# Optimization experiments

Hardware: AMD Instinct MI355X
Metric: run time of the kernel (lower is better)

Reference implementation:

```python
import jax, jax.numpy as jnp
import numpy as np

B, T, D, H = 2, 2048, 2048, 16
DH = D // H

def setup_inputs() -> dict:
    key = jax.random.key(0)
    k1, k2, k3 = jax.random.split(key, 3)
    x = jax.random.normal(k1, (B, T, D), dtype=jnp.float32)
    w_qkv = jax.random.normal(k2, (D, 3 * D), dtype=jnp.float32) * (1.0 / np.sqrt(D))
    w_o = jax.random.normal(k3, (D, D), dtype=jnp.float32) * (1.0 / np.sqrt(D))
    return {"x": x, "w_qkv": w_qkv, "w_o": w_o}

def reference(x, w_qkv, w_o):
    b, t, d = x.shape
    qkv = (x @ w_qkv).reshape(b, t, 3, H, DH)
    q, k, v = qkv[:, :, 0], qkv[:, :, 1], qkv[:, :, 2]  # [b,t,h,dh]
    scale = 1.0 / np.sqrt(DH).astype(np.float32)
    # scores: [b,h,t,t]
    scores = jnp.einsum('bqhd,bkhd->bhqk', q, k) * scale
    causal = jnp.tril(jnp.ones((t, t), dtype=bool))
    scores = jnp.where(causal[None, None], scores, -jnp.inf)
    attn = jax.nn.softmax(scores, axis=-1)
    out = jnp.einsum('bhqk,bkhd->bqhd', attn, v).reshape(b, t, d)
    return out @ w_o
```

## Files before the change

### kernel.cpp

```cpp
#include <hip/hip_runtime.h>
#include <hip/hip_bf16.h>

#define B_   2
#define T_   2048
#define D_   2048
#define H_   16
#define DH_  128
#define TD3_ 6144

typedef __attribute__((ext_vector_type(8))) short   short8;
typedef __attribute__((ext_vector_type(8))) unsigned short ushort8v;
typedef __attribute__((ext_vector_type(4))) float   f32x4;
typedef __attribute__((ext_vector_type(4))) float   f4v;
typedef __attribute__((ext_vector_type(4))) unsigned short u16x4;

static __device__ __forceinline__ unsigned short f2bf(float f) {
  unsigned int u = __builtin_bit_cast(unsigned int, f);
  u += 0x7FFFu + ((u >> 16) & 1u);
  return (unsigned short)(u >> 16);
}
static __device__ __forceinline__ float bf2f(unsigned short u) {
  return __builtin_bit_cast(float, (unsigned int)u << 16);
}

static __device__ __forceinline__ void gload_lds16(const unsigned short* g, unsigned short* l) {
  __builtin_amdgcn_global_load_lds((const __attribute__((address_space(1))) void*)g,
                                   (__attribute__((address_space(3))) void*)l, 16, 0, 0);
}

__global__ __launch_bounds__(256) void convert_f32_bf16(const float* __restrict__ X,
                                                        unsigned short* __restrict__ Y, int n4) {
  for (int i = blockIdx.x * blockDim.x + threadIdx.x; i < n4; i += gridDim.x * blockDim.x) {
    f4v v = ((const f4v*)X)[i];
    u16x4 o;
    o[0] = f2bf(v[0]); o[1] = f2bf(v[1]); o[2] = f2bf(v[2]); o[3] = f2bf(v[3]);
    ((u16x4*)Y)[i] = o;
  }
}

__global__ __launch_bounds__(256) void transpose_f32_bf16(const float* __restrict__ W,
                                                          unsigned short* __restrict__ WT,
                                                          int K, int N) {
  __shared__ float tile[32][33];
  int n0 = blockIdx.x * 32, k0 = blockIdx.y * 32;
  int tx = threadIdx.x & 31, ty = threadIdx.x >> 5;
#pragma unroll
  for (int r = 0; r < 4; r++)
    tile[ty + 8 * r][tx] = W[(size_t)(k0 + ty + 8 * r) * N + n0 + tx];
  __syncthreads();
#pragma unroll
  for (int r = 0; r < 4; r++)
    WT[(size_t)(n0 + ty + 8 * r) * K + k0 + tx] = f2bf(tile[tx][ty + 8 * r]);
}

__global__ __launch_bounds__(256) void vtr_kernel(const unsigned short* __restrict__ qkv,
                                                  unsigned short* __restrict__ vtg) {
  __shared__ unsigned short tile[64][68];
  const int t0 = blockIdx.x * 64;
  const int h = blockIdx.y >> 1, dh0 = (blockIdx.y & 1) * 64;
  const int b = blockIdx.z;
  const int tid = threadIdx.x;
  const unsigned short* src = qkv + (size_t)b * T_ * TD3_ + 2 * D_ + h * DH_ + dh0;
  {
    const int r = tid >> 3, cc = (tid & 7) * 8;
#pragma unroll
    for (int k = 0; k < 2; k++) {
      ushort8v v = *(const ushort8v*)(src + (size_t)(t0 + k * 32 + r) * TD3_ + cc);
      *(ushort8v*)&tile[k * 32 + r][cc] = v;
    }
  }
  __syncthreads();
  unsigned short* dst = vtg + ((size_t)(b * H_ + h) * DH_ + dh0) * T_ + t0;
  {
    const int d = tid >> 3, tc = (tid & 7) * 8;
#pragma unroll
    for (int k = 0; k < 2; k++) {
      ushort8v v;
#pragma unroll
      for (int j = 0; j < 8; j++) v[j] = tile[tc + j][k * 32 + d];
      *(ushort8v*)(dst + (size_t)(k * 32 + d) * T_ + tc) = v;
    }
  }
}

__global__ __launch_bounds__(512, 1) void gemm_qkv192(const unsigned short* __restrict__ A,
                                                      const unsigned short* __restrict__ BT,
                                                      unsigned short* __restrict__ C,
                                                      int M, int N, int K) {
  __shared__ unsigned short lA[2][2][128 * 64];
  __shared__ unsigned short lB[2][192 * 64];

  const int tid = threadIdx.x;
  const int bid = (int)blockIdx.x;
  const int npx = 4;
  const int xcd = bid & 7, idx = bid >> 3;
  const int n0 = (xcd * npx + (idx & 3)) * 192;
  const int m0 = (idx >> 2) * 256;
  const int l = tid & 63, lr = l & 15, lg = l >> 4;
  const int wid = tid >> 6, wm = wid >> 2, wn = wid & 3;
  const int nk = K >> 6;

  f32x4 acc[8][3] = {};
  short8 aQ0[4][2], aQ1[4][2], bX[3][2], bY[3][2];

  auto stageA = [&](int buf, int h, int kt) {
#pragma unroll
    for (int q = 0; q < 2; q++) {
      const int n = q * 512 + tid;
      const int row = n >> 3, ch = n & 7;
      gload_lds16(A + (size_t)(m0 + h * 128 + row) * K + kt * 64 + ((ch ^ (row & 7)) << 3),
                  &lA[buf][h][n * 8]);
    }
  };
  auto stageBt = [&](int buf, int third, int kt) {
    const int r = tid >> 3, ch = tid & 7;
    gload_lds16(BT + (size_t)(n0 + third * 64 + r) * K + kt * 64 + ((ch ^ (r & 7)) << 3),
                &lB[buf][third * 4096 + tid * 8]);
  };

#define QKV_STAGE_ALL(BUF, TT)                                                  \
  { stageA(BUF, 0, TT); stageA(BUF, 1, TT);                                     \
    stageBt(BUF, 0, TT); stageBt(BUF, 1, TT); stageBt(BUF, 2, TT); }

#define QKV_READ_A(DST, BUF, QUAD)                                              \
  _Pragma("unroll")                                                             \
  for (int mi = 0; mi < 4; mi++)                                                \
    _Pragma("unroll")                                                           \
    for (int kk = 0; kk < 2; kk++) {                                            \
      const int row = ((QUAD) * 4 + mi) * 16 + lr;                              \
      DST[mi][kk] = *(const short8*)&lA[BUF][wm][row * 64 +                     \
                      (((kk * 4 + lg) ^ (lr & 7)) << 3)];                       \
    }

#define QKV_READ_B(DST, BUF)                                                    \
  _Pragma("unroll")                                                             \
  for (int ni = 0; ni < 3; ni++)                                                \
    _Pragma("unroll")                                                           \
    for (int kk = 0; kk < 2; kk++) {                                            \
      const int row = wn * 48 + ni * 16 + lr;                                   \
      DST[ni][kk] = *(const short8*)&lB[BUF][row * 64 +                         \
                      (((kk * 4 + lg) ^ (lr & 7)) << 3)];                       \
    }

#define QKV_PHASE_A(BUF, BCUR, TT)                                              \
  {                                                                             \
    if ((TT) + 1 < nk) QKV_STAGE_ALL(1 - (BUF), (TT) + 1);                      \
    QKV_READ_A(aQ1, BUF, 1)                                                     \
    __builtin_amdgcn_s_setprio(1);                                              \
    _Pragma("unroll")                                                           \
    for (int mi = 0; mi < 4; mi++)                                              \
      _Pragma("unroll")                                                         \
      for (int ni = 0; ni < 3; ni++)                                            \
        _Pragma("unroll")                                                       \
        for (int kk = 0; kk < 2; kk++)                                          \
          acc[mi][ni] = __builtin_amdgcn_mfma_f32_16x16x32_bf16(                \
              aQ0[mi][kk], BCUR[ni][kk], acc[mi][ni], 0, 0, 0);                 \
    __builtin_amdgcn_s_setprio(0);                                              \
    __builtin_amdgcn_s_barrier();                                               \
  }

#define QKV_PHASE_B(BUF, BCUR, BNXT, TT)                                        \
  {                                                                             \
    __builtin_amdgcn_s_setprio(1);                                              \
    _Pragma("unroll")                                                           \
    for (int mi = 0; mi < 4; mi++)                                              \
      _Pragma("unroll")                                                         \
      for (int ni = 0; ni < 2; ni++)                                            \
        _Pragma("unroll")                                                       \
        for (int kk = 0; kk < 2; kk++)                                          \
          acc[4 + mi][ni] = __builtin_amdgcn_mfma_f32_16x16x32_bf16(            \
              aQ1[mi][kk], BCUR[ni][kk], acc[4 + mi][ni], 0, 0, 0);             \
    __builtin_amdgcn_s_setprio(0);                                              \
    asm volatile("s_waitcnt vmcnt(0)" ::: "memory");                            \
    __builtin_amdgcn_s_barrier();                                               \
    if ((TT) + 1 < nk) {                                                        \
      QKV_READ_A(aQ0, 1 - (BUF), 0)                                             \
      QKV_READ_B(BNXT, 1 - (BUF))                                               \
    }                                                                           \
    __builtin_amdgcn_s_setprio(1);                                              \
    _Pragma("unroll")                                                           \
    for (int mi = 0; mi < 4; mi++)                                              \
      _Pragma("unroll")                                                         \
      for (int kk = 0; kk < 2; kk++)                                            \
        acc[4 + mi][2] = __builtin_amdgcn_mfma_f32_16x16x32_bf16(               \
            aQ1[mi][kk], BCUR[2][kk], acc[4 + mi][2], 0, 0, 0);                 \
    __builtin_amdgcn_s_setprio(0);                                              \
    __builtin_amdgcn_s_barrier();                                               \
  }

  QKV_STAGE_ALL(0, 0)
  asm volatile("s_waitcnt vmcnt(0)" ::: "memory");
  __builtin_amdgcn_s_barrier();
  QKV_READ_A(aQ0, 0, 0)
  QKV_READ_B(bX, 0)

  for (int kt = 0; kt < nk; kt += 2) {
    QKV_PHASE_A(0, bX, kt)
    QKV_PHASE_B(0, bX, bY, kt)
    QKV_PHASE_A(1, bY, kt + 1)
    QKV_PHASE_B(1, bY, bX, kt + 1)
  }

#pragma unroll
  for (int mi = 0; mi < 8; mi++)
#pragma unroll
    for (int ni = 0; ni < 3; ni++)
#pragma unroll
      for (int i = 0; i < 4; i++) {
        const int row = m0 + wm * 128 + mi * 16 + lg * 4 + i;
        const int col = n0 + wn * 48 + ni * 16 + lr;
        C[(size_t)row * N + col] = f2bf(acc[mi][ni][i]);
      }
#undef QKV_PHASE_B
#undef QKV_PHASE_A
#undef QKV_READ_B
#undef QKV_READ_A
#undef QKV_STAGE_ALL
}

__global__ __launch_bounds__(512, 1) void gemm_op8(const unsigned short* __restrict__ A,
                                                   const unsigned short* __restrict__ BT,
                                                   float* __restrict__ C,
                                                   int M, int N, int K) {
  __shared__ unsigned short lA[2][128 * 64];
  __shared__ unsigned short lB[2][2][128 * 64];

  const int tid = threadIdx.x;
  const int bid = (int)blockIdx.x;
  const int xcd = bid & 7, idx = bid >> 3;
  const int n0 = xcd * 256, m0 = idx * 128;
  const int l = tid & 63, lr = l & 15, lg = l >> 4;
  const int wid = tid >> 6, wm = wid >> 2, wn = wid & 3;
  const int bh = wn >> 1, br0 = (wn & 1) * 64;
  const int nk = K >> 6;

  f32x4 acc[4][4] = {};

  auto stageA = [&](int buf, int kt) {
#pragma unroll
    for (int q = 0; q < 2; q++) {
      const int n = q * 512 + tid;
      const int row = n >> 3, ch = n & 7;
      gload_lds16(A + (size_t)(m0 + row) * K + kt * 64 + ((ch ^ (row & 7)) << 3),
                  &lA[buf][n * 8]);
    }
  };
  auto stageB = [&](int buf, int h, int kt) {
#pragma unroll
    for (int q = 0; q < 2; q++) {
      const int n = q * 512 + tid;
      const int row = n >> 3, ch = n & 7;
      gload_lds16(BT + (size_t)(n0 + h * 128 + row) * K + kt * 64 + ((ch ^ (row & 7)) << 3),
                  &lB[buf][h][n * 8]);
    }
  };

  stageB(0, 0, 0); stageB(0, 1, 0); stageA(0, 0);
  if (nk > 1) {
    stageB(1, 0, 1); stageB(1, 1, 1); stageA(1, 1);
    asm volatile("s_waitcnt vmcnt(6)" ::: "memory");
  } else {
    asm volatile("s_waitcnt vmcnt(0)" ::: "memory");
  }
  __builtin_amdgcn_s_barrier();

  short8 a[2][2], b0[2][2], b1[2][2];
  for (int kt = 0; kt < nk; kt++) {
    const int buf = kt & 1;

#pragma unroll
    for (int mi = 0; mi < 2; mi++)
#pragma unroll
      for (int kk = 0; kk < 2; kk++) {
        const int row = wm * 64 + mi * 16 + lr;
        a[mi][kk] = *(const short8*)&lA[buf][row * 64 + (((kk * 4 + lg) ^ (lr & 7)) << 3)];
      }
#pragma unroll
    for (int ni = 0; ni < 2; ni++)
#pragma unroll
      for (int kk = 0; kk < 2; kk++) {
        const int row = br0 + ni * 16 + lr;
        b0[ni][kk] = *(const short8*)&lB[buf][bh][row * 64 + (((kk * 4 + lg) ^ (lr & 7)) << 3)];
      }
    __builtin_amdgcn_s_barrier();
    __builtin_amdgcn_s_setprio(1);
#pragma unroll
    for (int mi = 0; mi < 2; mi++)
#pragma unroll
      for (int ni = 0; ni < 2; ni++)
#pragma unroll
        for (int kk = 0; kk < 2; kk++)
          acc[mi][ni] = __builtin_amdgcn_mfma_f32_16x16x32_bf16(a[mi][kk], b0[ni][kk], acc[mi][ni], 0, 0, 0);
    __builtin_amdgcn_s_setprio(0);
    __builtin_amdgcn_s_barrier();

#pragma unroll
    for (int ni = 0; ni < 2; ni++)
#pragma unroll
      for (int kk = 0; kk < 2; kk++) {
        const int row = br0 + (2 + ni) * 16 + lr;
        b1[ni][kk] = *(const short8*)&lB[buf][bh][row * 64 + (((kk * 4 + lg) ^ (lr & 7)) << 3)];
      }
    __builtin_amdgcn_s_barrier();
    __builtin_amdgcn_s_setprio(1);
#pragma unroll
    for (int mi = 0; mi < 2; mi++)
#pragma unroll
      for (int ni = 0; ni < 2; ni++)
#pragma unroll
        for (int kk = 0; kk < 2; kk++)
          acc[mi][2 + ni] = __builtin_amdgcn_mfma_f32_16x16x32_bf16(a[mi][kk], b1[ni][kk], acc[mi][2 + ni], 0, 0, 0);
    __builtin_amdgcn_s_setprio(0);
    __builtin_amdgcn_s_barrier();

#pragma unroll
    for (int mi = 0; mi < 2; mi++)
#pragma unroll
      for (int kk = 0; kk < 2; kk++) {
        const int row = wm * 64 + (2 + mi) * 16 + lr;
        a[mi][kk] = *(const short8*)&lA[buf][row * 64 + (((kk * 4 + lg) ^ (lr & 7)) << 3)];
      }
    if (kt + 2 < nk) stageB(buf, 0, kt + 2);
    __builtin_amdgcn_s_barrier();
    __builtin_amdgcn_s_setprio(1);
#pragma unroll
    for (int mi = 0; mi < 2; mi++)
#pragma unroll
      for (int ni = 0; ni < 2; ni++)
#pragma unroll
        for (int kk = 0; kk < 2; kk++)
          acc[2 + mi][2 + ni] = __builtin_amdgcn_mfma_f32_16x16x32_bf16(a[mi][kk], b1[ni][kk], acc[2 + mi][2 + ni], 0, 0, 0);
    __builtin_amdgcn_s_setprio(0);
    __builtin_amdgcn_s_barrier();

    if (kt + 2 < nk) { stageB(buf, 1, kt + 2); stageA(buf, kt + 2); }
    __builtin_amdgcn_s_barrier();
    __builtin_amdgcn_s_setprio(1);
#pragma unroll
    for (int mi = 0; mi < 2; mi++)
#pragma unroll
      for (int ni = 0; ni < 2; ni++)
#pragma unroll
        for (int kk = 0; kk < 2; kk++)
          acc[2 + mi][ni] = __builtin_amdgcn_mfma_f32_16x16x32_bf16(a[mi][kk], b0[ni][kk], acc[2 + mi][ni], 0, 0, 0);
    __builtin_amdgcn_s_setprio(0);
    if (kt + 2 < nk) asm volatile("s_waitcnt vmcnt(6)" ::: "memory");
    else             asm volatile("s_waitcnt vmcnt(0)" ::: "memory");
    __builtin_amdgcn_s_barrier();
  }

#pragma unroll
  for (int mi = 0; mi < 4; mi++)
#pragma unroll
    for (int ni = 0; ni < 4; ni++)
#pragma unroll
      for (int i = 0; i < 4; i++) {
        const int row = m0 + wm * 64 + mi * 16 + lg * 4 + i;
        const int col = n0 + wn * 64 + ni * 16 + lr;
        C[(size_t)row * N + col] = acc[mi][ni][i];
      }
}

__global__ __launch_bounds__(256, 2) void attn_fa(const unsigned short* __restrict__ qkv,
                                                  const unsigned short* __restrict__ vtg,
                                                  unsigned short* __restrict__ out) {
  const int x = blockIdx.x, h = blockIdx.y, b = blockIdx.z;
  const int qtl = b ? x : (T_ / 128 - 1 - x);
  const int q0 = qtl * 128;
  const int tid = threadIdx.x, w = tid >> 6, l = tid & 63, lr = l & 15, lg = l >> 4;

  const unsigned short* Qb = qkv + (size_t)b * T_ * TD3_ + h * DH_;
  const unsigned short* Kb = Qb + D_;
  const unsigned short* Vt = vtg + ((size_t)b * H_ + h) * DH_ * T_;

  __shared__ unsigned short klds[2][64 * 128];
  __shared__ unsigned short vt[2][128 * 64];
  __shared__ unsigned short plds[4][32 * 64];

  const float scale = 0.08838834764831845f;

  short8 qf[2][4];
#pragma unroll
  for (int mi = 0; mi < 2; mi++) {
    const unsigned short* qrow = Qb + (size_t)(q0 + w * 32 + mi * 16 + lr) * TD3_;
#pragma unroll
    for (int ks = 0; ks < 4; ks++) {
      ushort8v qv = *(const ushort8v*)(qrow + ks * 32 + lg * 8);
      short8 qs;
#pragma unroll
      for (int j = 0; j < 8; j++) qs[j] = (short)f2bf(bf2f(qv[j]) * scale);
      qf[mi][ks] = qs;
    }
  }

  f32x4 oacc[2][8] = {};
  float mrun[2][4], lsum[2][4];
#pragma unroll
  for (int mi = 0; mi < 2; mi++)
#pragma unroll
    for (int i = 0; i < 4; i++) { mrun[mi][i] = -__builtin_inff(); lsum[mi][i] = 0.f; }

  auto STAGE = [&](int buf, int kv0) {
#pragma unroll
    for (int it = 0; it < 4; it++) {
      const int n = it * 256 + tid;
      { const int kv = n >> 4, ch = n & 15;
        gload_lds16(Kb + (size_t)(kv0 + kv) * TD3_ + ((ch ^ (kv & 7)) << 3),
                    &klds[buf][n * 8]); }
      { const int dh = n >> 3, ch = n & 7;
        gload_lds16(Vt + (size_t)dh * T_ + kv0 + ((ch ^ (dh & 7)) << 3),
                    &vt[buf][n * 8]); }
    }
  };

  const int nt = 2 * qtl + 2;
  STAGE(0, 0);
  __syncthreads();

  for (int t = 0; t < nt; t++) {
    const int buf = t & 1;
    if (t + 1 < nt) STAGE(buf ^ 1, (t + 1) * 64);

    const int kv0 = t * 64;
    const bool active = (kv0 <= q0 + w * 32 + 31);
    if (active) {
      f32x4 s[2][4] = {};
      __builtin_amdgcn_s_setprio(1);
#pragma unroll
      for (int nf = 0; nf < 4; nf++) {
        const int kv = nf * 16 + lr;
#pragma unroll
        for (int ks = 0; ks < 4; ks++) {
          short8 kf = *(const short8*)&klds[buf][kv * 128 + (((ks * 4 + lg) ^ (lr & 7)) << 3)];
#pragma unroll
          for (int mi = 0; mi < 2; mi++)
            s[mi][nf] = __builtin_amdgcn_mfma_f32_16x16x32_bf16(qf[mi][ks], kf, s[mi][nf], 0, 0, 0);
        }
      }
      __builtin_amdgcn_s_setprio(0);

      const bool needmask = (kv0 + 63 > q0 + w * 32);
      float pmax[2][4];
#pragma unroll
      for (int mi = 0; mi < 2; mi++)
#pragma unroll
        for (int i = 0; i < 4; i++) pmax[mi][i] = -__builtin_inff();
#pragma unroll
      for (int mi = 0; mi < 2; mi++)
#pragma unroll
        for (int nf = 0; nf < 4; nf++)
#pragma unroll
          for (int i = 0; i < 4; i++) {
            float xv = s[mi][nf][i];
            if (needmask) {
              const int qr = w * 32 + mi * 16 + lg * 4 + i;
              const int kc = nf * 16 + lr;
              if (kv0 + kc > q0 + qr) xv = -__builtin_inff();
            }
            s[mi][nf][i] = xv;
            pmax[mi][i] = fmaxf(pmax[mi][i], xv);
          }
#pragma unroll
      for (int m = 1; m < 16; m <<= 1)
#pragma unroll
        for (int mi = 0; mi < 2; mi++)
#pragma unroll
          for (int i = 0; i < 4; i++) pmax[mi][i] = fmaxf(pmax[mi][i], __shfl_xor(pmax[mi][i], m));

      float alpha[2][4], rsum[2][4];
#pragma unroll
      for (int mi = 0; mi < 2; mi++)
#pragma unroll
        for (int i = 0; i < 4; i++) {
          const float mn = fmaxf(mrun[mi][i], pmax[mi][i]);
          alpha[mi][i] = __expf(mrun[mi][i] - mn);
          mrun[mi][i] = mn;
          rsum[mi][i] = 0.f;
        }
#pragma unroll
      for (int mi = 0; mi < 2; mi++)
#pragma unroll
        for (int nf = 0; nf < 4; nf++)
#pragma unroll
          for (int i = 0; i < 4; i++) {
            const float p = __expf(s[mi][nf][i] - mrun[mi][i]);
            rsum[mi][i] += p;
            const int prow = mi * 16 + lg * 4 + i;
            plds[w][prow * 64 + ((nf * 16 + lr) ^ ((prow & 7) << 3))] = f2bf(p);
          }
#pragma unroll
      for (int m = 1; m < 16; m <<= 1)
#pragma unroll
        for (int mi = 0; mi < 2; mi++)
#pragma unroll
          for (int i = 0; i < 4; i++) rsum[mi][i] += __shfl_xor(rsum[mi][i], m);
#pragma unroll
      for (int mi = 0; mi < 2; mi++)
#pragma unroll
        for (int i = 0; i < 4; i++) lsum[mi][i] = lsum[mi][i] * alpha[mi][i] + rsum[mi][i];
#pragma unroll
      for (int mi = 0; mi < 2; mi++)
#pragma unroll
        for (int nf = 0; nf < 8; nf++)
#pragma unroll
          for (int i = 0; i < 4; i++) oacc[mi][nf][i] *= alpha[mi][i];

      __builtin_amdgcn_s_setprio(1);
#pragma unroll
      for (int kk = 0; kk < 2; kk++) {
        short8 pa[2];
#pragma unroll
        for (int mi = 0; mi < 2; mi++) {
          const int prow = mi * 16 + lr;
          pa[mi] = *(const short8*)&plds[w][prow * 64 + (((kk * 32 + lg * 8)) ^ ((prow & 7) << 3))];
        }
#pragma unroll
        for (int nf = 0; nf < 8; nf++) {
          const short8 vb = *(const short8*)&vt[buf][(nf * 16 + lr) * 64 + (((kk * 4 + lg) ^ (lr & 7)) << 3)];
#pragma unroll
          for (int mi = 0; mi < 2; mi++)
            oacc[mi][nf] = __builtin_amdgcn_mfma_f32_16x16x32_bf16(pa[mi], vb, oacc[mi][nf], 0, 0, 0);
        }
      }
      __builtin_amdgcn_s_setprio(0);
    }
    __syncthreads();
  }

  float rinv[2][4];
#pragma unroll
  for (int mi = 0; mi < 2; mi++)
#pragma unroll
    for (int i = 0; i < 4; i++) rinv[mi][i] = 1.f / lsum[mi][i];
#pragma unroll
  for (int mi = 0; mi < 2; mi++) {
    unsigned short* orow = out + ((size_t)b * T_ + q0 + w * 32 + mi * 16 + lg * 4) * D_ + h * DH_;
#pragma unroll
    for (int nf = 0; nf < 8; nf++)
#pragma unroll
      for (int i = 0; i < 4; i++)
        orow[(size_t)i * D_ + nf * 16 + lr] = f2bf(oacc[mi][nf][i] * rinv[mi][i]);
  }
}

extern "C" void kernel_launch(void* const* d_in, const int* in_sizes, int n_in,
                              void* d_out, int out_size, void* d_ws, size_t ws_size,
                              hipStream_t stream) {
  const float* x    = (const float*)d_in[0];
  const float* wqkv = (const float*)d_in[1];
  const float* wo   = (const float*)d_in[2];
  float* out = (float*)d_out;

  char* ws = (char*)d_ws;
  unsigned short* xb    = (unsigned short*)(ws);
  unsigned short* wqkvt = (unsigned short*)(ws + 16777216);
  unsigned short* vtg   = (unsigned short*)(ws + 16777216);
  unsigned short* wot   = (unsigned short*)(ws + 41943040);
  unsigned short* qkv   = (unsigned short*)(ws + 50331648);
  unsigned short* attn  = xb;

  convert_f32_bf16<<<2048, 256, 0, stream>>>(x, xb, B_ * T_ * D_ / 4);
  transpose_f32_bf16<<<dim3(TD3_ / 32, D_ / 32), 256, 0, stream>>>(wqkv, wqkvt, D_, TD3_);
  transpose_f32_bf16<<<dim3(D_ / 32, D_ / 32), 256, 0, stream>>>(wo, wot, D_, D_);

  gemm_qkv192<<<dim3(512), 512, 0, stream>>>(xb, wqkvt, qkv, B_ * T_, TD3_, D_);
  vtr_kernel<<<dim3(T_ / 64, H_ * 2, B_), 256, 0, stream>>>(qkv, vtg);
  attn_fa<<<dim3(T_ / 128, H_, B_), 256, 0, stream>>>(qkv, vtg, attn);
  gemm_op8<<<dim3(256), 512, 0, stream>>>(attn, wot, out, B_ * T_, D_, D_);
}
```

Baseline: 284.8 us.

## Use exp2 softmax with lazy max rescaling and deferred row-sum reduction

Folds log2(e) into the Q pre-scale so the softmax can use the raw v_exp_f32 (exp2) instruction instead of __expf. Skips the cross-lane max reduction and the rescaling of the output accumulator whenever every lane's new tile max stays within 8 (in log2 units) of the running max. Row sums are now kept per lane and reduced across lanes only once after the KV loop, instead of on every tile. This trims shuffles, exponentials and accumulator multiplies in the attention inner loop. In exchange, unnormalised probabilities can reach up to 2^8 before conversion to bf16, and the wave-wide vote adds a branch.

```diff
diff --git a/kernel.cpp b/kernel.cpp
--- a/kernel.cpp
+++ b/kernel.cpp
@@ -21,6 +21,9 @@
 }
 static __device__ __forceinline__ float bf2f(unsigned short u) {
   return __builtin_bit_cast(float, (unsigned int)u << 16);
+}
+static __device__ __forceinline__ float fexp2(float x) {
+  float r; asm("v_exp_f32 %0, %1" : "=v"(r) : "v"(x)); return r;
 }
 
 static __device__ __forceinline__ void gload_lds16(const unsigned short* g, unsigned short* l) {
@@ -377,7 +380,7 @@
   __shared__ unsigned short vt[2][128 * 64];
   __shared__ unsigned short plds[4][32 * 64];
 
-  const float scale = 0.08838834764831845f;
+  const float scale2 = 0.12751744519764462f;
 
   short8 qf[2][4];
 #pragma unroll
@@ -388,17 +391,17 @@
       ushort8v qv = *(const ushort8v*)(qrow + ks * 32 + lg * 8);
       short8 qs;
 #pragma unroll
-      for (int j = 0; j < 8; j++) qs[j] = (short)f2bf(bf2f(qv[j]) * scale);
+      for (int j = 0; j < 8; j++) qs[j] = (short)f2bf(bf2f(qv[j]) * scale2);
       qf[mi][ks] = qs;
     }
   }
 
   f32x4 oacc[2][8] = {};
-  float mrun[2][4], lsum[2][4];
+  float mrun[2][4], rsuml[2][4];
 #pragma unroll
   for (int mi = 0; mi < 2; mi++)
 #pragma unroll
-    for (int i = 0; i < 4; i++) { mrun[mi][i] = -__builtin_inff(); lsum[mi][i] = 0.f; }
+    for (int i = 0; i < 4; i++) { mrun[mi][i] = -__builtin_inff(); rsuml[mi][i] = 0.f; }
 
   auto STAGE = [&](int buf, int kv0) {
 #pragma unroll
@@ -460,50 +463,46 @@
             s[mi][nf][i] = xv;
             pmax[mi][i] = fmaxf(pmax[mi][i], xv);
           }
-#pragma unroll
-      for (int m = 1; m < 16; m <<= 1)
+
+      int ok = 1;
+#pragma unroll
+      for (int mi = 0; mi < 2; mi++)
+#pragma unroll
+        for (int i = 0; i < 4; i++)
+          ok &= (pmax[mi][i] <= mrun[mi][i] + 8.0f) ? 1 : 0;
+
+      if (!__all(ok)) {
+#pragma unroll
+        for (int m = 1; m < 16; m <<= 1)
+#pragma unroll
+          for (int mi = 0; mi < 2; mi++)
+#pragma unroll
+            for (int i = 0; i < 4; i++)
+              pmax[mi][i] = fmaxf(pmax[mi][i], __shfl_xor(pmax[mi][i], m));
 #pragma unroll
         for (int mi = 0; mi < 2; mi++)
 #pragma unroll
-          for (int i = 0; i < 4; i++) pmax[mi][i] = fmaxf(pmax[mi][i], __shfl_xor(pmax[mi][i], m));
-
-      float alpha[2][4], rsum[2][4];
+          for (int i = 0; i < 4; i++) {
+            const float mn = fmaxf(mrun[mi][i], pmax[mi][i]);
+            const float al = fexp2(mrun[mi][i] - mn);
+            mrun[mi][i] = mn;
+            rsuml[mi][i] *= al;
+#pragma unroll
+            for (int nf = 0; nf < 8; nf++) oacc[mi][nf][i] *= al;
+          }
+      }
+
 #pragma unroll
       for (int mi = 0; mi < 2; mi++)
 #pragma unroll
-        for (int i = 0; i < 4; i++) {
-          const float mn = fmaxf(mrun[mi][i], pmax[mi][i]);
-          alpha[mi][i] = __expf(mrun[mi][i] - mn);
-          mrun[mi][i] = mn;
-          rsum[mi][i] = 0.f;
-        }
-#pragma unroll
-      for (int mi = 0; mi < 2; mi++)
-#pragma unroll
         for (int nf = 0; nf < 4; nf++)
 #pragma unroll
           for (int i = 0; i < 4; i++) {
-            const float p = __expf(s[mi][nf][i] - mrun[mi][i]);
-            rsum[mi][i] += p;
+            const float p = fexp2(s[mi][nf][i] - mrun[mi][i]);
+            rsuml[mi][i] += p;
             const int prow = mi * 16 + lg * 4 + i;
             plds[w][prow * 64 + ((nf * 16 + lr) ^ ((prow & 7) << 3))] = f2bf(p);
           }
-#pragma unroll
-      for (int m = 1; m < 16; m <<= 1)
-#pragma unroll
-        for (int mi = 0; mi < 2; mi++)
-#pragma unroll
-          for (int i = 0; i < 4; i++) rsum[mi][i] += __shfl_xor(rsum[mi][i], m);
-#pragma unroll
-      for (int mi = 0; mi < 2; mi++)
-#pragma unroll
-        for (int i = 0; i < 4; i++) lsum[mi][i] = lsum[mi][i] * alpha[mi][i] + rsum[mi][i];
-#pragma unroll
-      for (int mi = 0; mi < 2; mi++)
-#pragma unroll
-        for (int nf = 0; nf < 8; nf++)
-#pragma unroll
-          for (int i = 0; i < 4; i++) oacc[mi][nf][i] *= alpha[mi][i];
 
       __builtin_amdgcn_s_setprio(1);
 #pragma unroll
@@ -527,11 +526,18 @@
     __syncthreads();
   }
 
+#pragma unroll
+  for (int m = 1; m < 16; m <<= 1)
+#pragma unroll
+    for (int mi = 0; mi < 2; mi++)
+#pragma unroll
+      for (int i = 0; i < 4; i++) rsuml[mi][i] += __shfl_xor(rsuml[mi][i], m);
+
   float rinv[2][4];
 #pragma unroll
   for (int mi = 0; mi < 2; mi++)
 #pragma unroll
-    for (int i = 0; i < 4; i++) rinv[mi][i] = 1.f / lsum[mi][i];
+    for (int i = 0; i < 4; i++) rinv[mi][i] = 1.f / rsuml[mi][i];
 #pragma unroll
   for (int mi = 0; mi < 2; mi++) {
     unsigned short* orow = out + ((size_t)b * T_ + q0 + w * 32 + mi * 16 + lg * 4) * D_ + h * DH_;
```

Result: faster. 257.4 us (-9.6%).
